# Performance work log

Measured on AMD Instinct MI355X. Metric: run time of the kernel, lower is better.

## Reference

```python
import jax, jax.numpy as jnp
import numpy as np

NUM_EXPERTS = 8
HIDDEN = 2048
FFN = 4096
TOK_PER_EXPERT = 2048
TOTAL_TOKENS = NUM_EXPERTS * TOK_PER_EXPERT


def setup_inputs() -> dict:
    key = jax.random.key(0)
    kx, k1, k2 = jax.random.split(key, 3)
    permuted_hidden_states = jax.random.normal(kx, (TOTAL_TOKENS, HIDDEN), dtype=jnp.float32)
    # Linear weights stored torch-style [out_features, in_features]
    w1 = jax.random.normal(k1, (NUM_EXPERTS, 2 * FFN, HIDDEN), dtype=jnp.float32) * (1.0 / np.sqrt(HIDDEN))
    w2 = jax.random.normal(k2, (NUM_EXPERTS, HIDDEN, FFN), dtype=jnp.float32) * (1.0 / np.sqrt(FFN))
    tokens_per_expert = jnp.full((NUM_EXPERTS,), TOK_PER_EXPERT, dtype=jnp.int64)
    return {
        "permuted_hidden_states": permuted_hidden_states,
        "tokens_per_expert": tokens_per_expert,
        "w1": w1,
        "w2": w2,
    }


def _glu(x):
    a, b = jnp.split(x, 2, axis=-1)
    return jax.nn.silu(a) * b


def reference(permuted_hidden_states, tokens_per_expert, w1, w2):
    # tokens_per_expert is a concrete host-side int array (routing metadata),
    # matching the torch module where it drives Python-level slicing.
    counts = np.asarray(tokens_per_expert)
    outs = []
    start = 0
    for i in range(counts.shape[0]):
        n = int(counts[i])
        if n == 0:
            continue
        x = permuted_hidden_states[start:start + n]          # [n, H]
        fc1 = x @ w1[i].T                                     # [n, 2*F]
        inter = _glu(fc1)                                     # [n, F]
        outs.append(inter @ w2[i].T)                          # [n, H]
        start += n
    return jnp.concatenate(outs, axis=0)
```

## Files before the change

### kernel.cpp

```cpp
#include <hip/hip_runtime.h>

#define E_NUM 8
#define HID   2048
#define FFN_  4096
#define TOK   2048

typedef __attribute__((ext_vector_type(8))) short short8;
typedef __attribute__((ext_vector_type(4))) float f32x4;

__device__ __forceinline__ short f2bf(float f) {
  unsigned u = __builtin_bit_cast(unsigned, f);
  u += 0x7fffu + ((u >> 16) & 1u);
  return (short)(u >> 16);
}

__device__ __forceinline__ void gld_lds16(const void* g, void* l) {
  __builtin_amdgcn_global_load_lds(
      (const __attribute__((address_space(1))) void*)g,
      (__attribute__((address_space(3))) void*)l, 16, 0, 0);
}

__global__ __launch_bounds__(256) void cast_f32_bf16(const float* __restrict__ s,
                                                     short* __restrict__ d, long n) {
  long idx = ((long)blockIdx.x * 256 + threadIdx.x) * 8;
  long stride = (long)gridDim.x * 256 * 8;
  for (; idx < n; idx += stride) {
    float4 v0 = *(const float4*)(s + idx);
    float4 v1 = *(const float4*)(s + idx + 4);
    short8 o;
    o[0] = f2bf(v0.x); o[1] = f2bf(v0.y); o[2] = f2bf(v0.z); o[3] = f2bf(v0.w);
    o[4] = f2bf(v1.x); o[5] = f2bf(v1.y); o[6] = f2bf(v1.z); o[7] = f2bf(v1.w);
    *(short8*)(d + idx) = o;
  }
}

__global__ __launch_bounds__(256) void cast_w1_perm(const float* __restrict__ src,
                                                    short* __restrict__ dst) {
  int b = blockIdx.x;
  int e = b >> 13;
  int rp = b & 8191;
  int q = rp >> 5, h = (rp >> 4) & 1, i = rp & 15;
  int ro = h * FFN_ + q * 16 + i;
  const float* s = src + ((size_t)e * 8192 + ro) * HID + threadIdx.x * 8;
  short* d = dst + (size_t)b * HID + threadIdx.x * 8;
  float4 v0 = *(const float4*)s;
  float4 v1 = *(const float4*)(s + 4);
  short8 o;
  o[0] = f2bf(v0.x); o[1] = f2bf(v0.y); o[2] = f2bf(v0.z); o[3] = f2bf(v0.w);
  o[4] = f2bf(v1.x); o[5] = f2bf(v1.y); o[6] = f2bf(v1.z); o[7] = f2bf(v1.w);
  *(short8*)d = o;
}


__device__ __forceinline__ short8 frag_ld(const short* tile, int sub, int lane) {
  int lr = lane & 15;
  int c = ((lane >> 4) * 8) ^ ((lr & 8) << 1);
  return *(const short8*)((const char*)tile + sub * 1024 + lr * 64 + c * 2);
}

#define RD_A4(DST, BUF, H, S)                                     \
  _Pragma("unroll") for (int mf = 0; mf < 4; mf++)                \
      DST[mf] = frag_ld(BUF, (wm * 8 + (H) + mf) * 2 + (S), lane);

#define RD_B2(DST, BUF, BB, S)                                    \
  _Pragma("unroll") for (int nf = 0; nf < 2; nf++)                \
      DST[nf] = frag_ld(BUF, (wn * 4 + (BB) + nf) * 2 + (S), lane);

#define MFMA8(H, BC, AR, BR)                                      \
  _Pragma("unroll") for (int mf = 0; mf < 4; mf++)                \
  _Pragma("unroll") for (int nf = 0; nf < 2; nf++)                \
      acc[(H) + mf][(BC) + nf] = __builtin_amdgcn_mfma_f32_16x16x32_bf16( \
          AR[mf], BR[nf], acc[(H) + mf][(BC) + nf], 0, 0, 0);

#define STAGE(BASE, TILE, H, KO) do {                                               \
    gld_lds16((BASE) + (size_t)(H) * 128 * KDIM + (KO),                             \
              (TILE) + (((H) * 8 + w) * 2 + 0) * 512);                              \
    gld_lds16((BASE) + (size_t)(H) * 128 * KDIM + (KO) + 32,                        \
              (TILE) + (((H) * 8 + w) * 2 + 1) * 512);                              \
  } while (0)

#define BAR __builtin_amdgcn_s_barrier()
#define SB  __builtin_amdgcn_sched_barrier(0)
#define P1  __builtin_amdgcn_s_setprio(1)
#define P0  __builtin_amdgcn_s_setprio(0)
#define WT_LGKM0 __builtin_amdgcn_s_waitcnt(0xC07F)
#define WT_LGKM2 __builtin_amdgcn_s_waitcnt(0xC27F)
#define WT_LGKM4 __builtin_amdgcn_s_waitcnt(0xC47F)
#define WT_VM0   __builtin_amdgcn_s_waitcnt(0x3F70)
#define WT_VM4   __builtin_amdgcn_s_waitcnt(0x3F74)

#define TILE8(TAIL, KO, ASR, ASN, BSC, BSN) do {                           \
               \
  RD_B2(B1, BSC, 0, 0); SB; RD_A4(Ab, ASR, 0, 1);                          \
  if ((TAIL) < 2) STAGE(Agt, ASN, 0, (KO) + 64);                           \
  SB; WT_LGKM4; SB; P1; MFMA8(0, 0, Aa, B1); P0;                           \
                                                    \
  if ((TAIL) < 2) STAGE(Agt, ASN, 1, (KO) + 64);                           \
  SB; WT_LGKM0; SB; P1; MFMA8(0, 0, Ab, B2); P0;                           \
                                                    \
  SB; P1; MFMA8(0, 2, Ab, B3); P0;                                         \
                                 \
  RD_A4(Ab, ASR, 4, 0);                                                    \
  SB; P1; MFMA8(0, 2, Aa, B4); P0;                                         \
     \
  RD_A4(Aa, ASR, 4, 1);                                                    \
  SB;                                                                       \
  if ((TAIL) < 2) { WT_VM4; }                                              \
  BAR; WT_LGKM4; SB; P1; MFMA8(4, 2, Ab, B4); P0;                          \
                \
  if ((TAIL) < 2) RD_B2(B4, BSN, 2, 0);                                    \
  if ((TAIL) == 0) STAGE(Bgt, BSC, 0, (KO) + 128);                         \
  SB;                                                                       \
  if ((TAIL) < 2) { WT_LGKM2; } else { WT_LGKM0; }                         \
  SB; P1; MFMA8(4, 2, Aa, B3); P0;                                         \
                                \
  if ((TAIL) < 2) RD_B2(B3, BSN, 2, 1);                                    \
  if ((TAIL) == 0) STAGE(Bgt, BSC, 1, (KO) + 128);                         \
  SB;                                                                       \
  if ((TAIL) == 0) { WT_VM4; } else if ((TAIL) == 1) { WT_VM0; }           \
  BAR; SB; P1; MFMA8(4, 0, Aa, B2); P0;                                    \
               \
  if ((TAIL) < 2) { RD_A4(Aa, ASN, 0, 0); RD_B2(B2, BSN, 0, 1); }          \
  SB; P1; MFMA8(4, 0, Ab, B1); P0;                                         \
} while (0)

template <int KDIM, bool GLU>
__global__ __launch_bounds__(512, 2) void gemm256(const short* __restrict__ A,
                                                  const short* __restrict__ B,
                                                  void* __restrict__ C, int ldc) {
  constexpr int NT = KDIM / 64;
  const int e = blockIdx.z;
  const int m0 = blockIdx.y * 256;
  const int n0 = blockIdx.x * 256;
  const int N = gridDim.x * 256;
  const int tid = threadIdx.x;
  const int w = tid >> 6, lane = tid & 63;
  const int wm = w >> 2, wn = w & 3;

  const short* Ag = A + (size_t)e * TOK * KDIM + (size_t)m0 * KDIM;
  const short* Bg = B + (size_t)e * N * KDIM + (size_t)n0 * KDIM;

  __shared__ __align__(16) short As0[16384];
  __shared__ __align__(16) short As1[16384];
  __shared__ __align__(16) short Bs0[16384];
  __shared__ __align__(16) short Bs1[16384];

  f32x4 acc[8][4] = {};
  short8 Aa[4], Ab[4], B1[2], B2[2], B3[2], B4[2];

  const int slr = lane >> 2;
  const int sclog = ((lane & 3) * 8) ^ ((slr & 8) << 1);
  const short* Agt = Ag + (size_t)(w * 16 + slr) * KDIM + sclog;
  const short* Bgt = Bg + (size_t)(w * 16 + slr) * KDIM + sclog;

  STAGE(Bgt, Bs0, 0, 0); STAGE(Bgt, Bs0, 1, 0);
  STAGE(Agt, As0, 0, 0); STAGE(Agt, As0, 1, 0);
  STAGE(Bgt, Bs1, 0, 64); STAGE(Bgt, Bs1, 1, 64);
  WT_VM4; SB; BAR;
  RD_B2(B4, Bs0, 2, 0); SB;
  RD_B2(B3, Bs0, 2, 1); SB;
  RD_A4(Aa, As0, 0, 0); RD_B2(B2, Bs0, 0, 1); SB;

#pragma unroll 1
  for (int t = 0; t + 3 < NT; t += 2) {
    TILE8(0, t * 64, As0, As1, Bs0, Bs1);
    TILE8(0, (t + 1) * 64, As1, As0, Bs1, Bs0);
  }
  TILE8(1, (NT - 2) * 64, As0, As1, Bs0, Bs1);
  TILE8(2, (NT - 1) * 64, As1, As0, Bs1, Bs0);

  const int fq = lane >> 4, fr = lane & 15;
  if constexpr (GLU) {
    short* outp = (short*)C + (size_t)e * TOK * ldc;
    const int colb = (n0 >> 1) + wn * 32;
#pragma unroll
    for (int mf = 0; mf < 8; mf++)
#pragma unroll
      for (int p = 0; p < 2; p++)
#pragma unroll
        for (int r = 0; r < 4; r++) {
          int row = m0 + wm * 128 + mf * 16 + fq * 4 + r;
          int col = colb + p * 16 + fr;
          float av = acc[mf][2 * p][r];
          float bv = acc[mf][2 * p + 1][r];
          float sv = av / (1.0f + __expf(-av)) * bv;
          outp[(size_t)row * ldc + col] = f2bf(sv);
        }
  } else {
    float* outp = (float*)C + (size_t)e * TOK * ldc;
#pragma unroll
    for (int mf = 0; mf < 8; mf++)
#pragma unroll
      for (int nf = 0; nf < 4; nf++)
#pragma unroll
        for (int r = 0; r < 4; r++) {
          int row = m0 + wm * 128 + mf * 16 + fq * 4 + r;
          int col = n0 + wn * 64 + nf * 16 + fr;
          outp[(size_t)row * ldc + col] = acc[mf][nf][r];
        }
  }
}

extern "C" void kernel_launch(void* const* d_in, const int* in_sizes, int n_in,
                              void* d_out, int out_size, void* d_ws, size_t ws_size,
                              hipStream_t stream) {
  const float* x  = (const float*)d_in[0];
  const float* w1 = (const float*)d_in[2];
  const float* w2 = (const float*)d_in[3];

  const size_t W1P_BYTES   = (size_t)E_NUM * 2 * FFN_ * HID * 2;
  const size_t W2B_BYTES   = (size_t)E_NUM * HID * FFN_ * 2;
  const size_t INTER_BYTES = (size_t)E_NUM * TOK * FFN_ * 2;
  if (ws_size < W1P_BYTES + W2B_BYTES + INTER_BYTES) return;

  short* w1p   = (short*)d_ws;
  short* w2b   = (short*)((char*)d_ws + W1P_BYTES);
  short* inter = (short*)((char*)d_ws + W1P_BYTES + W2B_BYTES);
  short* xb    = (short*)d_out;
  float* out   = (float*)d_out;

  cast_f32_bf16<<<2048, 256, 0, stream>>>(x, xb, (long)E_NUM * TOK * HID);
  cast_f32_bf16<<<2048, 256, 0, stream>>>(w2, w2b, (long)E_NUM * HID * FFN_);
  cast_w1_perm<<<E_NUM * 8192, 256, 0, stream>>>(w1, w1p);

  gemm256<HID, true><<<dim3(32, 8, E_NUM), 512, 0, stream>>>(xb, w1p, (void*)inter, FFN_);
  gemm256<FFN_, false><<<dim3(8, 8, E_NUM), 512, 0, stream>>>(inter, w2b, (void*)out, HID);
}
```

Baseline: 932.2 us.

## Pad K-stride of second GEMM operands and restagger global-to-LDS loads

Pads the row stride of the bf16 w2 copy and the GLU intermediate from 4096 to 4128 elements, when the workspace is large enough, to reduce channel/bank conflicts from power-of-two strides in the second GEMM. A new row-wise cast kernel writes w2 into the padded layout. The GEMM pipeline is also reworked: each STAGE is split into two half-loads spread between MFMA groups, with an adjusted vmcnt wait, and pointers are advanced incrementally rather than indexed by K offset. The risk is extra workspace use and a changed wait-count schedule that could expose load latency.

```diff
diff --git a/kernel.cpp b/kernel.cpp
--- a/kernel.cpp
+++ b/kernel.cpp
@@ -31,6 +31,25 @@
     o[0] = f2bf(v0.x); o[1] = f2bf(v0.y); o[2] = f2bf(v0.z); o[3] = f2bf(v0.w);
     o[4] = f2bf(v1.x); o[5] = f2bf(v1.y); o[6] = f2bf(v1.z); o[7] = f2bf(v1.w);
     *(short8*)(d + idx) = o;
+  }
+}
+
+__global__ __launch_bounds__(256) void cast_rows4096(const float* __restrict__ s,
+                                                     short* __restrict__ d,
+                                                     int ldd, long nrows) {
+  long idx = (long)blockIdx.x * 256 + threadIdx.x;
+  long stride = (long)gridDim.x * 256;
+  long nchunk = nrows * 512;
+  for (; idx < nchunk; idx += stride) {
+    long row = idx >> 9;
+    int c = (int)(idx & 511) * 8;
+    const float* sp = s + row * 4096 + c;
+    float4 v0 = *(const float4*)sp;
+    float4 v1 = *(const float4*)(sp + 4);
+    short8 o;
+    o[0] = f2bf(v0.x); o[1] = f2bf(v0.y); o[2] = f2bf(v0.z); o[3] = f2bf(v0.w);
+    o[4] = f2bf(v1.x); o[5] = f2bf(v1.y); o[6] = f2bf(v1.z); o[7] = f2bf(v1.w);
+    *(short8*)(d + (size_t)row * ldd + c) = o;
   }
 }
 
@@ -72,11 +91,13 @@
       acc[(H) + mf][(BC) + nf] = __builtin_amdgcn_mfma_f32_16x16x32_bf16( \
           AR[mf], BR[nf], acc[(H) + mf][(BC) + nf], 0, 0, 0);
 
-#define STAGE(BASE, TILE, H, KO) do {                                               \
-    gld_lds16((BASE) + (size_t)(H) * 128 * KDIM + (KO),                             \
-              (TILE) + (((H) * 8 + w) * 2 + 0) * 512);                              \
-    gld_lds16((BASE) + (size_t)(H) * 128 * KDIM + (KO) + 32,                        \
-              (TILE) + (((H) * 8 + w) * 2 + 1) * 512);                              \
+#define STAGE0(BASE, TILE, KOFF) do {                                   \
+    gld_lds16((BASE) + (KOFF),      (TILE) + (w * 2 + 0) * 512);        \
+    gld_lds16((BASE) + (KOFF) + 32, (TILE) + (w * 2 + 1) * 512);        \
+  } while (0)
+#define STAGE1(BASE, TILE, KOFF) do {                                   \
+    gld_lds16((BASE) + h1off + (KOFF),      (TILE) + ((8 + w) * 2 + 0) * 512); \
+    gld_lds16((BASE) + h1off + (KOFF) + 32, (TILE) + ((8 + w) * 2 + 1) * 512); \
   } while (0)
 
 #define BAR __builtin_amdgcn_s_barrier()
@@ -87,18 +108,21 @@
 #define WT_LGKM2 __builtin_amdgcn_s_waitcnt(0xC27F)
 #define WT_LGKM4 __builtin_amdgcn_s_waitcnt(0xC47F)
 #define WT_VM0   __builtin_amdgcn_s_waitcnt(0x3F70)
+#define WT_VM2   __builtin_amdgcn_s_waitcnt(0x3F72)
 #define WT_VM4   __builtin_amdgcn_s_waitcnt(0x3F74)
 
-#define TILE8(TAIL, KO, ASR, ASN, BSC, BSN) do {                           \
-               \
+#define TILE8(TAIL, KB, ASR, ASN, BSC, BSN) do {                           \
+   \
   RD_B2(B1, BSC, 0, 0); SB; RD_A4(Ab, ASR, 0, 1);                          \
-  if ((TAIL) < 2) STAGE(Agt, ASN, 0, (KO) + 64);                           \
-  SB; WT_LGKM4; SB; P1; MFMA8(0, 0, Aa, B1); P0;                           \
+  SB; WT_LGKM4; SB; P1; MFMA8(0, 0, Aa, B1); P0; SB;                       \
+  if ((TAIL) < 2) STAGE0(Agt, ASN, (KB) + 64);                             \
+  SB;                                                                       \
+                                  \
+  WT_LGKM0; SB; P1; MFMA8(0, 0, Ab, B2); P0; SB;                           \
+  if ((TAIL) < 2) STAGE1(Agt, ASN, (KB) + 64);                             \
+  SB;                                                                       \
                                                     \
-  if ((TAIL) < 2) STAGE(Agt, ASN, 1, (KO) + 64);                           \
-  SB; WT_LGKM0; SB; P1; MFMA8(0, 0, Ab, B2); P0;                           \
-                                                    \
-  SB; P1; MFMA8(0, 2, Ab, B3); P0;                                         \
+  P1; MFMA8(0, 2, Ab, B3); P0;                                             \
                                  \
   RD_A4(Ab, ASR, 4, 0);                                                    \
   SB; P1; MFMA8(0, 2, Aa, B4); P0;                                         \
@@ -107,28 +131,31 @@
   SB;                                                                       \
   if ((TAIL) < 2) { WT_VM4; }                                              \
   BAR; WT_LGKM4; SB; P1; MFMA8(4, 2, Ab, B4); P0;                          \
-                \
+          \
   if ((TAIL) < 2) RD_B2(B4, BSN, 2, 0);                                    \
-  if ((TAIL) == 0) STAGE(Bgt, BSC, 0, (KO) + 128);                         \
   SB;                                                                       \
   if ((TAIL) < 2) { WT_LGKM2; } else { WT_LGKM0; }                         \
-  SB; P1; MFMA8(4, 2, Aa, B3); P0;                                         \
-                                \
+  SB; P1; MFMA8(4, 2, Aa, B3); P0; SB;                                     \
+  if ((TAIL) == 0) STAGE0(Bgt, BSC, (KB) + 128);                           \
+  SB;                                                                       \
+                                        \
   if ((TAIL) < 2) RD_B2(B3, BSN, 2, 1);                                    \
-  if ((TAIL) == 0) STAGE(Bgt, BSC, 1, (KO) + 128);                         \
-  SB;                                                                       \
-  if ((TAIL) == 0) { WT_VM4; } else if ((TAIL) == 1) { WT_VM0; }           \
-  BAR; SB; P1; MFMA8(4, 0, Aa, B2); P0;                                    \
+  SB;                                                                       \
+  if ((TAIL) == 0) { WT_VM2; } else if ((TAIL) == 1) { WT_VM0; }           \
+  BAR; SB; P1; MFMA8(4, 0, Aa, B2); P0; SB;                                \
+  if ((TAIL) == 0) STAGE1(Bgt, BSC, (KB) + 128);                           \
+  SB;                                                                       \
                \
   if ((TAIL) < 2) { RD_A4(Aa, ASN, 0, 0); RD_B2(B2, BSN, 0, 1); }          \
   SB; P1; MFMA8(4, 0, Ab, B1); P0;                                         \
 } while (0)
 
-template <int KDIM, bool GLU>
+template <int KLEN, bool GLU>
 __global__ __launch_bounds__(512, 2) void gemm256(const short* __restrict__ A,
                                                   const short* __restrict__ B,
-                                                  void* __restrict__ C, int ldc) {
-  constexpr int NT = KDIM / 64;
+                                                  void* __restrict__ C,
+                                                  int ldc, int ld) {
+  constexpr int NT = KLEN / 64;
   const int e = blockIdx.z;
   const int m0 = blockIdx.y * 256;
   const int n0 = blockIdx.x * 256;
@@ -137,8 +164,8 @@
   const int w = tid >> 6, lane = tid & 63;
   const int wm = w >> 2, wn = w & 3;
 
-  const short* Ag = A + (size_t)e * TOK * KDIM + (size_t)m0 * KDIM;
-  const short* Bg = B + (size_t)e * N * KDIM + (size_t)n0 * KDIM;
+  const short* Ag = A + (size_t)e * TOK * ld + (size_t)m0 * ld;
+  const short* Bg = B + (size_t)e * N * ld + (size_t)n0 * ld;
 
   __shared__ __align__(16) short As0[16384];
   __shared__ __align__(16) short As1[16384];
@@ -150,12 +177,13 @@
 
   const int slr = lane >> 2;
   const int sclog = ((lane & 3) * 8) ^ ((slr & 8) << 1);
-  const short* Agt = Ag + (size_t)(w * 16 + slr) * KDIM + sclog;
-  const short* Bgt = Bg + (size_t)(w * 16 + slr) * KDIM + sclog;
-
-  STAGE(Bgt, Bs0, 0, 0); STAGE(Bgt, Bs0, 1, 0);
-  STAGE(Agt, As0, 0, 0); STAGE(Agt, As0, 1, 0);
-  STAGE(Bgt, Bs1, 0, 64); STAGE(Bgt, Bs1, 1, 64);
+  const short* Agt = Ag + (size_t)(w * 16 + slr) * ld + sclog;
+  const short* Bgt = Bg + (size_t)(w * 16 + slr) * ld + sclog;
+  const size_t h1off = (size_t)128 * ld;
+
+  STAGE0(Bgt, Bs0, 0); STAGE1(Bgt, Bs0, 0);
+  STAGE0(Agt, As0, 0); STAGE1(Agt, As0, 0);
+  STAGE0(Bgt, Bs1, 64); STAGE1(Bgt, Bs1, 64);
   WT_VM4; SB; BAR;
   RD_B2(B4, Bs0, 2, 0); SB;
   RD_B2(B3, Bs0, 2, 1); SB;
@@ -163,11 +191,12 @@
 
 #pragma unroll 1
   for (int t = 0; t + 3 < NT; t += 2) {
-    TILE8(0, t * 64, As0, As1, Bs0, Bs1);
-    TILE8(0, (t + 1) * 64, As1, As0, Bs1, Bs0);
-  }
-  TILE8(1, (NT - 2) * 64, As0, As1, Bs0, Bs1);
-  TILE8(2, (NT - 1) * 64, As1, As0, Bs1, Bs0);
+    TILE8(0, 0, As0, As1, Bs0, Bs1);
+    TILE8(0, 64, As1, As0, Bs1, Bs0);
+    Agt += 128; Bgt += 128;
+  }
+  TILE8(1, 0, As0, As1, Bs0, Bs1);
+  TILE8(2, 64, As1, As0, Bs1, Bs0);
 
   const int fq = lane >> 4, fr = lane & 15;
   if constexpr (GLU) {
@@ -208,9 +237,14 @@
   const float* w1 = (const float*)d_in[2];
   const float* w2 = (const float*)d_in[3];
 
-  const size_t W1P_BYTES   = (size_t)E_NUM * 2 * FFN_ * HID * 2;
-  const size_t W2B_BYTES   = (size_t)E_NUM * HID * FFN_ * 2;
-  const size_t INTER_BYTES = (size_t)E_NUM * TOK * FFN_ * 2;
+  const size_t W1P_BYTES = (size_t)E_NUM * 2 * FFN_ * HID * 2;
+  const int PAD_LD = FFN_ + 32;
+  const size_t W2B_PAD   = (size_t)E_NUM * HID * PAD_LD * 2;
+  const size_t INTER_PAD = (size_t)E_NUM * TOK * PAD_LD * 2;
+  int ldK2 = (ws_size >= W1P_BYTES + W2B_PAD + INTER_PAD) ? PAD_LD : FFN_;
+
+  const size_t W2B_BYTES   = (size_t)E_NUM * HID * ldK2 * 2;
+  const size_t INTER_BYTES = (size_t)E_NUM * TOK * ldK2 * 2;
   if (ws_size < W1P_BYTES + W2B_BYTES + INTER_BYTES) return;
 
   short* w1p   = (short*)d_ws;
@@ -220,9 +254,11 @@
   float* out   = (float*)d_out;
 
   cast_f32_bf16<<<2048, 256, 0, stream>>>(x, xb, (long)E_NUM * TOK * HID);
-  cast_f32_bf16<<<2048, 256, 0, stream>>>(w2, w2b, (long)E_NUM * HID * FFN_);
+  cast_rows4096<<<2048, 256, 0, stream>>>(w2, w2b, ldK2, (long)E_NUM * HID);
   cast_w1_perm<<<E_NUM * 8192, 256, 0, stream>>>(w1, w1p);
 
-  gemm256<HID, true><<<dim3(32, 8, E_NUM), 512, 0, stream>>>(xb, w1p, (void*)inter, FFN_);
-  gemm256<FFN_, false><<<dim3(8, 8, E_NUM), 512, 0, stream>>>(inter, w2b, (void*)out, HID);
-}
+  gemm256<HID, true><<<dim3(32, 8, E_NUM), 512, 0, stream>>>(
+      xb, w1p, (void*)inter, ldK2, HID);
+  gemm256<FFN_, false><<<dim3(8, 8, E_NUM), 512, 0, stream>>>(
+      inter, w2b, (void*)out, HID, ldK2);
+}
```

After: 1.031 ms. +10.6%, slower.
